# Kernel tuning notes

Measured on AMD Instinct MI355X. Metric: run time of the kernel, lower is better.

Reference implementation:

```python
import jax, jax.numpy as jnp
import numpy as np

N = 400_000      # active sparse voxels
C = 128          # hidden_size
GRID = 128       # dense grid extent per axis
KVOL = 27        # 3x3x3 kernel offsets


def _build_kmap():
    """Build a consistent neighbor map (the 'kmap') from random sparse voxel coords."""
    rng = np.random.default_rng(0)
    lin = np.sort(rng.choice(GRID ** 3, size=N, replace=False).astype(np.int64))
    lookup = np.full(GRID ** 3, -1, dtype=np.int32)
    lookup[lin] = np.arange(N, dtype=np.int32)
    x = lin // (GRID * GRID)
    y = (lin // GRID) % GRID
    z = lin % GRID
    nbr = np.full((N, KVOL), -1, dtype=np.int32)
    k = 0
    for dx in (-1, 0, 1):
        for dy in (-1, 0, 1):
            for dz in (-1, 0, 1):
                nx, ny, nz = x + dx, y + dy, z + dz
                valid = (nx >= 0) & (nx < GRID) & (ny >= 0) & (ny < GRID) & \
                        (nz >= 0) & (nz < GRID)
                nlin = (nx * GRID + ny) * GRID + nz
                nbr[:, k] = np.where(valid, lookup[np.clip(nlin, 0, GRID ** 3 - 1)], -1)
                k += 1
    return nbr


def setup_inputs() -> dict:
    key = jax.random.key(0)
    ks = jax.random.split(key, 6)
    s = 1.0 / np.sqrt(C)
    return {
        "feats": jax.random.normal(ks[0], (N, C), jnp.float32),
        "neighbor_idx": jnp.asarray(_build_kmap()),
        "conv_w": jax.random.normal(ks[1], (KVOL, C, C), jnp.float32) * (s / np.sqrt(KVOL)),
        "conv_b": jax.random.normal(ks[2], (C,), jnp.float32) * 0.01,
        "lin_w": jax.random.normal(ks[3], (C, C), jnp.float32) * s,   # torch Linear weight [out,in]
        "lin_b": jax.random.normal(ks[4], (C,), jnp.float32) * 0.01,
        "ln_g": jnp.ones((C,), jnp.float32),
        "ln_b": jnp.zeros((C,), jnp.float32),
    }


def reference(feats, neighbor_idx, conv_w, conv_b, lin_w, lin_b, ln_g, ln_b):
    # --- sparse 3x3x3 conv via kmap gather-GEMM-accumulate ---
    out = jnp.zeros_like(feats)
    for k in range(KVOL):  # fixed small structural loop over kernel offsets
        idx = neighbor_idx[:, k]
        valid = (idx >= 0)[:, None]
        gathered = jnp.where(valid, feats[jnp.maximum(idx, 0)], 0.0)  # [N, C]
        out = out + gathered @ conv_w[k]
    out = out + conv_b                      # conv bias add on jagged data
    # --- Linear (torch: x @ W.T + b) ---
    out = out @ lin_w.T + lin_b
    # --- LayerNorm over channel dim (eps=1e-5) ---
    mu = jnp.mean(out, axis=-1, keepdims=True)
    var = jnp.mean(jnp.square(out - mu), axis=-1, keepdims=True)
    out = (out - mu) * jax.lax.rsqrt(var + 1e-5) * ln_g + ln_b
    return out
```

## Files before the change

kernel.cpp:

```cpp
#include <hip/hip_runtime.h>

typedef __bf16 bf16;
typedef unsigned short u16;
typedef __attribute__((ext_vector_type(8))) __bf16 bf16x8;
typedef __attribute__((ext_vector_type(4))) float f32x4;
typedef const __attribute__((address_space(1))) char gchar;
typedef const __attribute__((address_space(1))) bf16x8 gbf16x8;

#define N_PTS 400000
#define KVOL 27
#define SCHED0() __builtin_amdgcn_sched_barrier(0)

__device__ __forceinline__ f32x4 mfma16(bf16x8 a, bf16x8 b, f32x4 c) {
  return __builtin_amdgcn_mfma_f32_16x16x32_bf16(a, b, c, 0, 0, 0);
}

__global__ __launch_bounds__(256) void cast_feats_k(const float4* __restrict__ in,
                                                    bf16x8* __restrict__ out) {
  int i = blockIdx.x * 256 + threadIdx.x;
  float4 a = in[2 * i], b = in[2 * i + 1];
  bf16x8 v;
  v[0] = (bf16)a.x; v[1] = (bf16)a.y; v[2] = (bf16)a.z; v[3] = (bf16)a.w;
  v[4] = (bf16)b.x; v[5] = (bf16)b.y; v[6] = (bf16)b.z; v[7] = (bf16)b.w;
  out[i] = v;
}

__global__ __launch_bounds__(256) void cast_w2_k(const float* __restrict__ conv_w,
                                                 const float* __restrict__ lin_w,
                                                 const float* __restrict__ conv_b,
                                                 const float* __restrict__ lin_b,
                                                 bf16x8* __restrict__ wt2,
                                                 float* __restrict__ b2,
                                                 bf16x8* __restrict__ zrow) {
  int t = blockIdx.x * 256 + threadIdx.x;
  if (t < KVOL * 2048) {
    int lane = t & 63;
    int ct = (t >> 6) & 7;
    int kf = (t >> 9) & 3;
    int k = t >> 11;
    int co = ct * 16 + (lane & 15);
    int ci0 = kf * 32 + (lane >> 4) * 8;
    float s[8];
#pragma unroll
    for (int j = 0; j < 8; ++j) s[j] = 0.f;
    const float4* lw = (const float4*)(lin_w + (size_t)co * 128);
    for (int c4 = 0; c4 < 32; ++c4) {
      float4 w = lw[c4];
#pragma unroll
      for (int j = 0; j < 8; ++j) {
        float4 cv = *(const float4*)(conv_w + ((size_t)(k * 128 + ci0 + j)) * 128 + c4 * 4);
        s[j] += cv.x * w.x + cv.y * w.y + cv.z * w.z + cv.w * w.w;
      }
    }
    bf16x8 v;
#pragma unroll
    for (int j = 0; j < 8; ++j) v[j] = (bf16)s[j];
    wt2[t] = v;
  } else if (t < KVOL * 2048 + 128) {
    int co = t - KVOL * 2048;
    float s = lin_b[co];
    for (int c = 0; c < 128; ++c) s += conv_b[c] * lin_w[(size_t)co * 128 + c];
    b2[co] = s;
  } else if (t < KVOL * 2048 + 128 + 16) {
    bf16x8 v = {};
    zrow[t - (KVOL * 2048 + 128)] = v;
  }
}

__global__ __launch_bounds__(256, 3) void fused_k(
    const bf16* __restrict__ featsb,
    const int* __restrict__ nbr,
    const bf16* __restrict__ wt2,
    const float* __restrict__ b2,
    const bf16* __restrict__ zrow,
    const float* __restrict__ ln_g,
    const float* __restrict__ ln_b,
    float* __restrict__ out) {
  __shared__ __align__(16) u16 wdb[2][8192];

  const int tid = threadIdx.x;
  const int lane = tid & 63;
  const int wv = tid >> 6;
  const int l15 = lane & 15;
  const int l4 = lane >> 4;

  const int nwg = gridDim.x;
  const int bid0 = blockIdx.x;
  const int q = nwg >> 3, r8 = nwg & 7;
  const int xcd = bid0 & 7, lo = bid0 >> 3;
  const int bid = (xcd < r8 ? xcd * (q + 1) : r8 * (q + 1) + (xcd - r8) * q) + lo;

  const int row0 = bid * 128;
  const int rb = row0 + wv * 32 + l15;
  const int aoff = l4 * 16;

  f32x4 acc[2][8];
#pragma unroll
  for (int rg = 0; rg < 2; ++rg)
#pragma unroll
    for (int ct = 0; ct < 8; ++ct) acc[rg][ct] = (f32x4)0.f;

  bf16x8 a[2][4];
  int idx_nxt[2], idx_n2[2];
  gchar* nb[2];

  auto stagef = [&](int ph, int buf) {
#pragma unroll
    for (int c = 0; c < 4; ++c) {
      const char* g = (const char*)wt2 + ((size_t)ph << 14) + c * 4096 + tid * 16;
      char* l = (char*)&wdb[buf][0] + c * 4096 + wv * 1024;
      __builtin_amdgcn_global_load_lds(
          (const __attribute__((address_space(1))) void*)g,
          (__attribute__((address_space(3))) void*)l, 16, 0, 0);
    }
  };

  auto mfma_pair = [&](int buf, int kfa) {
#pragma unroll
    for (int kh = 0; kh < 2; ++kh) {
      const int kf = kfa + kh;
      const u16* bp = &wdb[buf][0] + kh * 4096 + lane * 8;
      bf16x8 bfr[8];
#pragma unroll
      for (int ct = 0; ct < 8; ++ct) bfr[ct] = *(const bf16x8*)(bp + ct * 512);
      __builtin_amdgcn_s_setprio(1);
#pragma unroll
      for (int ct = 0; ct < 8; ++ct)
#pragma unroll
        for (int rg = 0; rg < 2; ++rg)
          acc[rg][ct] = mfma16(a[rg][kf], bfr[ct], acc[rg][ct]);
      __builtin_amdgcn_s_setprio(0);
#pragma unroll
      for (int rg = 0; rg < 2; ++rg)
        a[rg][kf] = *(gbf16x8*)(nb[rg] + kf * 64);
    }
  };

  {
    int idx0[2];
#pragma unroll
    for (int rg = 0; rg < 2; ++rg)
      idx0[rg] = nbr[(size_t)(rb + rg * 16) * KVOL + 0];
#pragma unroll
    for (int rg = 0; rg < 2; ++rg) {
      gchar* base = ((idx0[rg] < 0) ? (gchar*)zrow
                                    : (gchar*)featsb + (size_t)idx0[rg] * 256) + aoff;
#pragma unroll
      for (int kf = 0; kf < 4; ++kf) a[rg][kf] = *(gbf16x8*)(base + kf * 64);
    }
#pragma unroll
    for (int rg = 0; rg < 2; ++rg)
      idx_nxt[rg] = nbr[(size_t)(rb + rg * 16) * KVOL + 1];
  }
  stagef(0, 0);
  SCHED0();
  asm volatile("s_waitcnt vmcnt(0)" ::: "memory");
  SCHED0();
  __builtin_amdgcn_s_barrier();
  SCHED0();

  for (int t = 0; t < KVOL; ++t) {
    stagef(2 * t + 1, 1);
    SCHED0();
    {
      int kk = (t + 2 < KVOL) ? t + 2 : KVOL - 1;
#pragma unroll
      for (int rg = 0; rg < 2; ++rg)
        idx_n2[rg] = nbr[(size_t)(rb + rg * 16) * KVOL + kk];
    }
    SCHED0();
#pragma unroll
    for (int rg = 0; rg < 2; ++rg)
      nb[rg] = ((idx_nxt[rg] < 0) ? (gchar*)zrow
                                  : (gchar*)featsb + (size_t)idx_nxt[rg] * 256) + aoff;
    mfma_pair(0, 0);
    SCHED0();
    asm volatile("s_waitcnt vmcnt(6)" ::: "memory");
    SCHED0();
    __builtin_amdgcn_s_barrier();
    SCHED0();

    if (t < KVOL - 1) stagef(2 * t + 2, 0);
    SCHED0();
    mfma_pair(1, 2);
    SCHED0();
    asm volatile("s_waitcnt vmcnt(4)" ::: "memory");
    SCHED0();
    __builtin_amdgcn_s_barrier();
    SCHED0();

#pragma unroll
    for (int rg = 0; rg < 2; ++rg) idx_nxt[rg] = idx_n2[rg];
  }

  SCHED0();
  asm volatile("s_waitcnt vmcnt(0)" ::: "memory");
  SCHED0();

  float bv[8], lg[8], lb[8];
#pragma unroll
  for (int ct = 0; ct < 8; ++ct) {
    int c = ct * 16 + l15;
    bv[ct] = b2[c]; lg[ct] = ln_g[c]; lb[ct] = ln_b[c];
  }
#pragma unroll
  for (int rg = 0; rg < 2; ++rg) {
#pragma unroll
    for (int j = 0; j < 4; ++j) {
      float s = 0.f, qq = 0.f;
#pragma unroll
      for (int ct = 0; ct < 8; ++ct) {
        float x = acc[rg][ct][j] + bv[ct];
        s += x; qq += x * x;
      }
#pragma unroll
      for (int m = 1; m <= 8; m <<= 1) {
        s += __shfl_xor(s, m, 64);
        qq += __shfl_xor(qq, m, 64);
      }
      float mu = s * (1.f / 128.f);
      float var = qq * (1.f / 128.f) - mu * mu;
      float rstd = rsqrtf(var + 1e-5f);
      int r = row0 + wv * 32 + rg * 16 + l4 * 4 + j;
#pragma unroll
      for (int ct = 0; ct < 8; ++ct) {
        float x = acc[rg][ct][j] + bv[ct];
        out[(size_t)r * 128 + ct * 16 + l15] = (x - mu) * rstd * lg[ct] + lb[ct];
      }
    }
  }
}

extern "C" void kernel_launch(void* const* d_in, const int* in_sizes, int n_in,
                              void* d_out, int out_size, void* d_ws, size_t ws_size,
                              hipStream_t stream) {
  const float* feats  = (const float*)d_in[0];
  const int*   nbr    = (const int*)d_in[1];
  const float* conv_w = (const float*)d_in[2];
  const float* conv_b = (const float*)d_in[3];
  const float* lin_w  = (const float*)d_in[4];
  const float* lin_b  = (const float*)d_in[5];
  const float* ln_g   = (const float*)d_in[6];
  const float* ln_b   = (const float*)d_in[7];
  float* out = (float*)d_out;

  bf16* featsb = (bf16*)d_ws;
  bf16* wt2 = featsb + (size_t)N_PTS * 128;
  float* b2 = (float*)(wt2 + (size_t)KVOL * 128 * 128);
  bf16* zrow = (bf16*)(b2 + 128);

  cast_feats_k<<<25000, 256, 0, stream>>>((const float4*)feats, (bf16x8*)featsb);
  cast_w2_k<<<217, 256, 0, stream>>>(conv_w, lin_w, conv_b, lin_b,
                                     (bf16x8*)wt2, b2, (bf16x8*)zrow);
  fused_k<<<3125, 256, 0, stream>>>(featsb, nbr, wt2, b2, zrow, ln_g, ln_b, out);
}
```

Measured before the change: 388.8 us.

## Retile fused sparse conv waves to 64 rows by 64 cols with cross-wave LayerNorm

Each wave now computes a 64-row by 64-column tile instead of 32 rows by all 128 columns. This halves the per-wave LDS weight fragment reads and doubles the number of gathered feature rows each wave keeps in flight. Feature gathers use 32-bit offsets from featsb, and invalid neighbours point at a fixed zero-row offset (ZOFF), so the separate zrow pointer and 64-bit address math go away. LayerNorm statistics now need a cross-wave reduction through LDS with an extra barrier. The gather data is split into half-K register stages, which brings a new load-wait schedule.

```diff
diff --git a/kernel.cpp b/kernel.cpp
--- a/kernel.cpp
+++ b/kernel.cpp
@@ -2,6 +2,7 @@
 
 typedef __bf16 bf16;
 typedef unsigned short u16;
+typedef unsigned int u32;
 typedef __attribute__((ext_vector_type(8))) __bf16 bf16x8;
 typedef __attribute__((ext_vector_type(4))) float f32x4;
 typedef const __attribute__((address_space(1))) char gchar;
@@ -10,6 +11,7 @@
 #define N_PTS 400000
 #define KVOL 27
 #define SCHED0() __builtin_amdgcn_sched_barrier(0)
+#define ZOFF 103285248u
 
 __device__ __forceinline__ f32x4 mfma16(bf16x8 a, bf16x8 b, f32x4 c) {
   return __builtin_amdgcn_mfma_f32_16x16x32_bf16(a, b, c, 0, 0, 0);
@@ -72,7 +74,6 @@
     const int* __restrict__ nbr,
     const bf16* __restrict__ wt2,
     const float* __restrict__ b2,
-    const bf16* __restrict__ zrow,
     const float* __restrict__ ln_g,
     const float* __restrict__ ln_b,
     float* __restrict__ out) {
@@ -81,6 +82,8 @@
   const int tid = threadIdx.x;
   const int lane = tid & 63;
   const int wv = tid >> 6;
+  const int wr = wv >> 1;
+  const int wc = wv & 1;
   const int l15 = lane & 15;
   const int l4 = lane >> 4;
 
@@ -91,18 +94,18 @@
   const int bid = (xcd < r8 ? xcd * (q + 1) : r8 * (q + 1) + (xcd - r8) * q) + lo;
 
   const int row0 = bid * 128;
-  const int rb = row0 + wv * 32 + l15;
-  const int aoff = l4 * 16;
-
-  f32x4 acc[2][8];
-#pragma unroll
-  for (int rg = 0; rg < 2; ++rg)
-#pragma unroll
-    for (int ct = 0; ct < 8; ++ct) acc[rg][ct] = (f32x4)0.f;
-
-  bf16x8 a[2][4];
-  int idx_nxt[2], idx_n2[2];
-  gchar* nb[2];
+  const int rbl = row0 + wr * 64 + l15;
+  const u32 aoff = (u32)(l4 * 16);
+
+  f32x4 acc[4][4];
+#pragma unroll
+  for (int rg = 0; rg < 4; ++rg)
+#pragma unroll
+    for (int ctl = 0; ctl < 4; ++ctl) acc[rg][ctl] = (f32x4)0.f;
+
+  bf16x8 sA[4][2];
+  int idx_nxt[4], idx_n2[4];
+  u32 nbc[4], nbn[4];
 
   auto stagef = [&](int ph, int buf) {
 #pragma unroll
@@ -115,42 +118,42 @@
     }
   };
 
-  auto mfma_pair = [&](int buf, int kfa) {
+  auto mfma_half = [&](int buf, const u32* roff, int kbase) {
 #pragma unroll
     for (int kh = 0; kh < 2; ++kh) {
-      const int kf = kfa + kh;
-      const u16* bp = &wdb[buf][0] + kh * 4096 + lane * 8;
-      bf16x8 bfr[8];
-#pragma unroll
-      for (int ct = 0; ct < 8; ++ct) bfr[ct] = *(const bf16x8*)(bp + ct * 512);
+      const u16* bp = &wdb[buf][0] + kh * 4096 + (wc * 4) * 512 + lane * 8;
+      bf16x8 bfr[4];
+#pragma unroll
+      for (int ctl = 0; ctl < 4; ++ctl) bfr[ctl] = *(const bf16x8*)(bp + ctl * 512);
       __builtin_amdgcn_s_setprio(1);
 #pragma unroll
-      for (int ct = 0; ct < 8; ++ct)
-#pragma unroll
-        for (int rg = 0; rg < 2; ++rg)
-          acc[rg][ct] = mfma16(a[rg][kf], bfr[ct], acc[rg][ct]);
+      for (int ctl = 0; ctl < 4; ++ctl)
+#pragma unroll
+        for (int rg = 0; rg < 4; ++rg)
+          acc[rg][ctl] = mfma16(sA[rg][kh], bfr[ctl], acc[rg][ctl]);
       __builtin_amdgcn_s_setprio(0);
 #pragma unroll
-      for (int rg = 0; rg < 2; ++rg)
-        a[rg][kf] = *(gbf16x8*)(nb[rg] + kf * 64);
+      for (int rg = 0; rg < 4; ++rg)
+        sA[rg][kh] = *(gbf16x8*)((gchar*)featsb + roff[rg] + (u32)((kbase + kh) * 64));
     }
   };
 
   {
-    int idx0[2];
-#pragma unroll
-    for (int rg = 0; rg < 2; ++rg)
-      idx0[rg] = nbr[(size_t)(rb + rg * 16) * KVOL + 0];
-#pragma unroll
-    for (int rg = 0; rg < 2; ++rg) {
-      gchar* base = ((idx0[rg] < 0) ? (gchar*)zrow
-                                    : (gchar*)featsb + (size_t)idx0[rg] * 256) + aoff;
-#pragma unroll
-      for (int kf = 0; kf < 4; ++kf) a[rg][kf] = *(gbf16x8*)(base + kf * 64);
-    }
-#pragma unroll
-    for (int rg = 0; rg < 2; ++rg)
-      idx_nxt[rg] = nbr[(size_t)(rb + rg * 16) * KVOL + 1];
+    int idx0[4];
+#pragma unroll
+    for (int rg = 0; rg < 4; ++rg)
+      idx0[rg] = nbr[(size_t)(rbl + rg * 16) * KVOL + 0];
+#pragma unroll
+    for (int rg = 0; rg < 4; ++rg)
+      nbc[rg] = (idx0[rg] < 0 ? ZOFF : (u32)idx0[rg] * 256u) + aoff;
+#pragma unroll
+    for (int rg = 0; rg < 4; ++rg)
+#pragma unroll
+      for (int kh = 0; kh < 2; ++kh)
+        sA[rg][kh] = *(gbf16x8*)((gchar*)featsb + nbc[rg] + (u32)(kh * 64));
+#pragma unroll
+    for (int rg = 0; rg < 4; ++rg)
+      idx_nxt[rg] = nbr[(size_t)(rbl + rg * 16) * KVOL + 1];
   }
   stagef(0, 0);
   SCHED0();
@@ -165,52 +168,55 @@
     {
       int kk = (t + 2 < KVOL) ? t + 2 : KVOL - 1;
 #pragma unroll
-      for (int rg = 0; rg < 2; ++rg)
-        idx_n2[rg] = nbr[(size_t)(rb + rg * 16) * KVOL + kk];
-    }
-    SCHED0();
-#pragma unroll
-    for (int rg = 0; rg < 2; ++rg)
-      nb[rg] = ((idx_nxt[rg] < 0) ? (gchar*)zrow
-                                  : (gchar*)featsb + (size_t)idx_nxt[rg] * 256) + aoff;
-    mfma_pair(0, 0);
-    SCHED0();
-    asm volatile("s_waitcnt vmcnt(6)" ::: "memory");
+      for (int rg = 0; rg < 4; ++rg)
+        idx_n2[rg] = nbr[(size_t)(rbl + rg * 16) * KVOL + kk];
+    }
+    SCHED0();
+    mfma_half(0, nbc, 2);
+    SCHED0();
+    asm volatile("s_waitcnt vmcnt(12)" ::: "memory");
     SCHED0();
     __builtin_amdgcn_s_barrier();
     SCHED0();
 
     if (t < KVOL - 1) stagef(2 * t + 2, 0);
     SCHED0();
-    mfma_pair(1, 2);
-    SCHED0();
-    asm volatile("s_waitcnt vmcnt(4)" ::: "memory");
+#pragma unroll
+    for (int rg = 0; rg < 4; ++rg)
+      nbn[rg] = (idx_nxt[rg] < 0 ? ZOFF : (u32)idx_nxt[rg] * 256u) + aoff;
+    mfma_half(1, nbn, 0);
+    SCHED0();
+    asm volatile("s_waitcnt vmcnt(8)" ::: "memory");
     SCHED0();
     __builtin_amdgcn_s_barrier();
     SCHED0();
 
 #pragma unroll
-    for (int rg = 0; rg < 2; ++rg) idx_nxt[rg] = idx_n2[rg];
+    for (int rg = 0; rg < 4; ++rg) { nbc[rg] = nbn[rg]; idx_nxt[rg] = idx_n2[rg]; }
   }
 
   SCHED0();
   asm volatile("s_waitcnt vmcnt(0)" ::: "memory");
   SCHED0();
-
-  float bv[8], lg[8], lb[8];
-#pragma unroll
-  for (int ct = 0; ct < 8; ++ct) {
-    int c = ct * 16 + l15;
-    bv[ct] = b2[c]; lg[ct] = ln_g[c]; lb[ct] = ln_b[c];
-  }
-#pragma unroll
-  for (int rg = 0; rg < 2; ++rg) {
+  __builtin_amdgcn_s_barrier();
+  SCHED0();
+
+  float* red = (float*)&wdb[0][0];
+  float bv[4], lg[4], lb[4];
+#pragma unroll
+  for (int ctl = 0; ctl < 4; ++ctl) {
+    int c = wc * 64 + ctl * 16 + l15;
+    bv[ctl] = b2[c]; lg[ctl] = ln_g[c]; lb[ctl] = ln_b[c];
+  }
+  float smy[4][4], qmy[4][4];
+#pragma unroll
+  for (int rg = 0; rg < 4; ++rg) {
 #pragma unroll
     for (int j = 0; j < 4; ++j) {
       float s = 0.f, qq = 0.f;
 #pragma unroll
-      for (int ct = 0; ct < 8; ++ct) {
-        float x = acc[rg][ct][j] + bv[ct];
+      for (int ctl = 0; ctl < 4; ++ctl) {
+        float x = acc[rg][ctl][j] + bv[ctl];
         s += x; qq += x * x;
       }
 #pragma unroll
@@ -218,14 +224,31 @@
         s += __shfl_xor(s, m, 64);
         qq += __shfl_xor(qq, m, 64);
       }
-      float mu = s * (1.f / 128.f);
-      float var = qq * (1.f / 128.f) - mu * mu;
+      smy[rg][j] = s; qmy[rg][j] = qq;
+      if (l15 == 0) {
+        int rl = wr * 64 + rg * 16 + l4 * 4 + j;
+        red[(wc * 128 + rl) * 2 + 0] = s;
+        red[(wc * 128 + rl) * 2 + 1] = qq;
+      }
+    }
+  }
+  __syncthreads();
+#pragma unroll
+  for (int rg = 0; rg < 4; ++rg) {
+#pragma unroll
+    for (int j = 0; j < 4; ++j) {
+      int rl = wr * 64 + rg * 16 + l4 * 4 + j;
+      float so = red[((wc ^ 1) * 128 + rl) * 2 + 0];
+      float qo = red[((wc ^ 1) * 128 + rl) * 2 + 1];
+      float S = smy[rg][j] + so, Q = qmy[rg][j] + qo;
+      float mu = S * (1.f / 128.f);
+      float var = Q * (1.f / 128.f) - mu * mu;
       float rstd = rsqrtf(var + 1e-5f);
-      int r = row0 + wv * 32 + rg * 16 + l4 * 4 + j;
-#pragma unroll
-      for (int ct = 0; ct < 8; ++ct) {
-        float x = acc[rg][ct][j] + bv[ct];
-        out[(size_t)r * 128 + ct * 16 + l15] = (x - mu) * rstd * lg[ct] + lb[ct];
+      int r = row0 + rl;
+#pragma unroll
+      for (int ctl = 0; ctl < 4; ++ctl) {
+        float x = acc[rg][ctl][j] + bv[ctl];
+        out[(size_t)r * 128 + wc * 64 + ctl * 16 + l15] = (x - mu) * rstd * lg[ctl] + lb[ctl];
       }
     }
   }
@@ -252,5 +275,5 @@
   cast_feats_k<<<25000, 256, 0, stream>>>((const float4*)feats, (bf16x8*)featsb);
   cast_w2_k<<<217, 256, 0, stream>>>(conv_w, lin_w, conv_b, lin_b,
                                      (bf16x8*)wt2, b2, (bf16x8*)zrow);
-  fused_k<<<3125, 256, 0, stream>>>(featsb, nbr, wt2, b2, zrow, ln_g, ln_b, out);
-}
+  fused_k<<<3125, 256, 0, stream>>>(featsb, nbr, wt2, b2, ln_g, ln_b, out);
+}
```

Measured after the change: 546.7 us. +40.6%, slower.

## Switch fused sparse conv to 32x32x16 bf16 MFMA tiles

Applied to the files above, without the earlier changes.

Replaces the 16x16x32 MFMA tiling (two 16-row groups per wave, eight column tiles) with 32x32x16 MFMAs (one 32-row group, four column tiles). The weight pre-packing layout, the per-lane gather addressing (one neighbor index per lane instead of two) and the LayerNorm epilogue lane mapping all change to match. This cuts LDS B-fragment reads and the number of gather address computations per wave, at the cost of a different wait-count schedule and longer-latency MFMA instructions.

```diff
diff --git a/kernel.cpp b/kernel.cpp
--- a/kernel.cpp
+++ b/kernel.cpp
@@ -3,7 +3,7 @@
 typedef __bf16 bf16;
 typedef unsigned short u16;
 typedef __attribute__((ext_vector_type(8))) __bf16 bf16x8;
-typedef __attribute__((ext_vector_type(4))) float f32x4;
+typedef __attribute__((ext_vector_type(16))) float f32x16;
 typedef const __attribute__((address_space(1))) char gchar;
 typedef const __attribute__((address_space(1))) bf16x8 gbf16x8;
 
@@ -11,8 +11,8 @@
 #define KVOL 27
 #define SCHED0() __builtin_amdgcn_sched_barrier(0)
 
-__device__ __forceinline__ f32x4 mfma16(bf16x8 a, bf16x8 b, f32x4 c) {
-  return __builtin_amdgcn_mfma_f32_16x16x32_bf16(a, b, c, 0, 0, 0);
+__device__ __forceinline__ f32x16 mfma32(bf16x8 a, bf16x8 b, f32x16 c) {
+  return __builtin_amdgcn_mfma_f32_32x32x16_bf16(a, b, c, 0, 0, 0);
 }
 
 __global__ __launch_bounds__(256) void cast_feats_k(const float4* __restrict__ in,
@@ -35,11 +35,11 @@
   int t = blockIdx.x * 256 + threadIdx.x;
   if (t < KVOL * 2048) {
     int lane = t & 63;
-    int ct = (t >> 6) & 7;
-    int kf = (t >> 9) & 3;
+    int ct = (t >> 6) & 3;
+    int ik = (t >> 8) & 7;
     int k = t >> 11;
-    int co = ct * 16 + (lane & 15);
-    int ci0 = kf * 32 + (lane >> 4) * 8;
+    int co = ct * 32 + (lane & 31);
+    int ci0 = ik * 16 + (lane >> 5) * 8;
     float s[8];
 #pragma unroll
     for (int j = 0; j < 8; ++j) s[j] = 0.f;
@@ -81,8 +81,8 @@
   const int tid = threadIdx.x;
   const int lane = tid & 63;
   const int wv = tid >> 6;
-  const int l15 = lane & 15;
-  const int l4 = lane >> 4;
+  const int l31 = lane & 31;
+  const int lh = lane >> 5;
 
   const int nwg = gridDim.x;
   const int bid0 = blockIdx.x;
@@ -91,18 +91,16 @@
   const int bid = (xcd < r8 ? xcd * (q + 1) : r8 * (q + 1) + (xcd - r8) * q) + lo;
 
   const int row0 = bid * 128;
-  const int rb = row0 + wv * 32 + l15;
-  const int aoff = l4 * 16;
-
-  f32x4 acc[2][8];
-#pragma unroll
-  for (int rg = 0; rg < 2; ++rg)
-#pragma unroll
-    for (int ct = 0; ct < 8; ++ct) acc[rg][ct] = (f32x4)0.f;
-
-  bf16x8 a[2][4];
-  int idx_nxt[2], idx_n2[2];
-  gchar* nb[2];
+  const int myrow = row0 + wv * 32 + l31;
+  const int aoff = lh * 16;
+
+  f32x16 acc[4];
+#pragma unroll
+  for (int ct = 0; ct < 4; ++ct) acc[ct] = (f32x16)0.f;
+
+  bf16x8 a[8];
+  int idx_nxt, idx_n2;
+  gchar* nb;
 
   auto stagef = [&](int ph, int buf) {
 #pragma unroll
@@ -115,42 +113,29 @@
     }
   };
 
-  auto mfma_pair = [&](int buf, int kfa) {
-#pragma unroll
-    for (int kh = 0; kh < 2; ++kh) {
-      const int kf = kfa + kh;
-      const u16* bp = &wdb[buf][0] + kh * 4096 + lane * 8;
-      bf16x8 bfr[8];
-#pragma unroll
-      for (int ct = 0; ct < 8; ++ct) bfr[ct] = *(const bf16x8*)(bp + ct * 512);
+  auto mfma_half = [&](int buf, int kbase) {
+#pragma unroll
+    for (int ik = 0; ik < 4; ++ik) {
+      const int c = kbase + ik;
+      const u16* bp = &wdb[buf][0] + ik * 2048 + lane * 8;
+      bf16x8 bfr[4];
+#pragma unroll
+      for (int ct = 0; ct < 4; ++ct) bfr[ct] = *(const bf16x8*)(bp + ct * 512);
       __builtin_amdgcn_s_setprio(1);
 #pragma unroll
-      for (int ct = 0; ct < 8; ++ct)
-#pragma unroll
-        for (int rg = 0; rg < 2; ++rg)
-          acc[rg][ct] = mfma16(a[rg][kf], bfr[ct], acc[rg][ct]);
+      for (int ct = 0; ct < 4; ++ct) acc[ct] = mfma32(a[c], bfr[ct], acc[ct]);
       __builtin_amdgcn_s_setprio(0);
-#pragma unroll
-      for (int rg = 0; rg < 2; ++rg)
-        a[rg][kf] = *(gbf16x8*)(nb[rg] + kf * 64);
+      a[c] = *(gbf16x8*)(nb + c * 32);
     }
   };
 
   {
-    int idx0[2];
-#pragma unroll
-    for (int rg = 0; rg < 2; ++rg)
-      idx0[rg] = nbr[(size_t)(rb + rg * 16) * KVOL + 0];
-#pragma unroll
-    for (int rg = 0; rg < 2; ++rg) {
-      gchar* base = ((idx0[rg] < 0) ? (gchar*)zrow
-                                    : (gchar*)featsb + (size_t)idx0[rg] * 256) + aoff;
-#pragma unroll
-      for (int kf = 0; kf < 4; ++kf) a[rg][kf] = *(gbf16x8*)(base + kf * 64);
-    }
-#pragma unroll
-    for (int rg = 0; rg < 2; ++rg)
-      idx_nxt[rg] = nbr[(size_t)(rb + rg * 16) * KVOL + 1];
+    int idx0 = nbr[(size_t)myrow * KVOL + 0];
+    gchar* base = ((idx0 < 0) ? (gchar*)zrow
+                              : (gchar*)featsb + (size_t)idx0 * 256) + aoff;
+#pragma unroll
+    for (int c = 0; c < 8; ++c) a[c] = *(gbf16x8*)(base + c * 32);
+    idx_nxt = nbr[(size_t)myrow * KVOL + 1];
   }
   stagef(0, 0);
   SCHED0();
@@ -164,69 +149,61 @@
     SCHED0();
     {
       int kk = (t + 2 < KVOL) ? t + 2 : KVOL - 1;
-#pragma unroll
-      for (int rg = 0; rg < 2; ++rg)
-        idx_n2[rg] = nbr[(size_t)(rb + rg * 16) * KVOL + kk];
-    }
-    SCHED0();
-#pragma unroll
-    for (int rg = 0; rg < 2; ++rg)
-      nb[rg] = ((idx_nxt[rg] < 0) ? (gchar*)zrow
-                                  : (gchar*)featsb + (size_t)idx_nxt[rg] * 256) + aoff;
-    mfma_pair(0, 0);
-    SCHED0();
-    asm volatile("s_waitcnt vmcnt(6)" ::: "memory");
+      idx_n2 = nbr[(size_t)myrow * KVOL + kk];
+    }
+    SCHED0();
+    nb = ((idx_nxt < 0) ? (gchar*)zrow
+                        : (gchar*)featsb + (size_t)idx_nxt * 256) + aoff;
+    mfma_half(0, 0);
+    SCHED0();
+    asm volatile("s_waitcnt vmcnt(5)" ::: "memory");
     SCHED0();
     __builtin_amdgcn_s_barrier();
     SCHED0();
 
     if (t < KVOL - 1) stagef(2 * t + 2, 0);
     SCHED0();
-    mfma_pair(1, 2);
+    mfma_half(1, 4);
     SCHED0();
     asm volatile("s_waitcnt vmcnt(4)" ::: "memory");
     SCHED0();
     __builtin_amdgcn_s_barrier();
     SCHED0();
 
-#pragma unroll
-    for (int rg = 0; rg < 2; ++rg) idx_nxt[rg] = idx_n2[rg];
+    idx_nxt = idx_n2;
   }
 
   SCHED0();
   asm volatile("s_waitcnt vmcnt(0)" ::: "memory");
   SCHED0();
 
-  float bv[8], lg[8], lb[8];
-#pragma unroll
-  for (int ct = 0; ct < 8; ++ct) {
-    int c = ct * 16 + l15;
+  float bv[4], lg[4], lb[4];
+#pragma unroll
+  for (int ct = 0; ct < 4; ++ct) {
+    int c = ct * 32 + l31;
     bv[ct] = b2[c]; lg[ct] = ln_g[c]; lb[ct] = ln_b[c];
   }
 #pragma unroll
-  for (int rg = 0; rg < 2; ++rg) {
-#pragma unroll
-    for (int j = 0; j < 4; ++j) {
-      float s = 0.f, qq = 0.f;
-#pragma unroll
-      for (int ct = 0; ct < 8; ++ct) {
-        float x = acc[rg][ct][j] + bv[ct];
-        s += x; qq += x * x;
-      }
-#pragma unroll
-      for (int m = 1; m <= 8; m <<= 1) {
-        s += __shfl_xor(s, m, 64);
-        qq += __shfl_xor(qq, m, 64);
-      }
-      float mu = s * (1.f / 128.f);
-      float var = qq * (1.f / 128.f) - mu * mu;
-      float rstd = rsqrtf(var + 1e-5f);
-      int r = row0 + wv * 32 + rg * 16 + l4 * 4 + j;
-#pragma unroll
-      for (int ct = 0; ct < 8; ++ct) {
-        float x = acc[rg][ct][j] + bv[ct];
-        out[(size_t)r * 128 + ct * 16 + l15] = (x - mu) * rstd * lg[ct] + lb[ct];
-      }
+  for (int reg = 0; reg < 16; ++reg) {
+    float s = 0.f, qq = 0.f;
+#pragma unroll
+    for (int ct = 0; ct < 4; ++ct) {
+      float x = acc[ct][reg] + bv[ct];
+      s += x; qq += x * x;
+    }
+#pragma unroll
+    for (int m = 1; m <= 16; m <<= 1) {
+      s += __shfl_xor(s, m, 64);
+      qq += __shfl_xor(qq, m, 64);
+    }
+    float mu = s * (1.f / 128.f);
+    float var = qq * (1.f / 128.f) - mu * mu;
+    float rstd = rsqrtf(var + 1e-5f);
+    int r = row0 + wv * 32 + (reg & 3) + 8 * (reg >> 2) + 4 * lh;
+#pragma unroll
+    for (int ct = 0; ct < 4; ++ct) {
+      float x = acc[ct][reg] + bv[ct];
+      out[(size_t)r * 128 + ct * 32 + l31] = (x - mu) * rstd * lg[ct] + lb[ct];
     }
   }
 }
```

Measured after the change: 421.0 us. 8.3% more time.
